# Kernel optimization log

Measured on AMD Instinct MI355X. Metric: run time of the kernel, lower is better.

## Reference

```python
import jax, jax.numpy as jnp
import numpy as np
import itertools

# Fixed 3x5 signal matrix from the module
_M = jnp.array([[1., 0., 0., 0., 0.],
                [0., 0., 1., 1., -1.],
                [0., 1., 0., -1., 1.]], dtype=jnp.float32)
# All 6 permutations of 3 elements (itertools order, matching torch code)
_PERM = jnp.array(list(itertools.permutations(range(3))), dtype=jnp.int32)  # [6,3]

B, DIN, G = 8192, 3072, 1024  # dout = 3*G = 3072


def setup_inputs() -> dict:
    key = jax.random.key(0)
    k1, k2, k3, k4 = jax.random.split(key, 4)
    x = jax.random.normal(k1, (B, DIN), dtype=jnp.float32)
    connections = jax.random.randint(k2, (G, 3), 0, DIN)  # int indices into din
    selector = jax.random.normal(k3, (G, 3), dtype=jnp.float32)
    wgts = jax.random.normal(k4, (G, 6), dtype=jnp.float32)
    return {"x": x, "connections": connections, "selector": selector, "wgts": wgts}


def reference(x, connections, selector, wgts):
    # 1. gather 3 inputs per gate: [B, G, 3]
    inputs = jnp.take(x, connections, axis=1)
    # 2. soft selector blend (training path)
    C = selector / (1.0 + jnp.abs(selector))           # [G, 3]
    absC = jnp.abs(C)
    gated = (1.0 - absC)[None] * inputs + ((C + absC) * 0.5)[None]  # [B, G, 3]
    # 3-4. all 6 permutations of the 3 gate inputs: [B, G, 6, 3]
    p = gated[:, :, _PERM]
    # 5. interaction columns -> [B, G, 6, 5]
    feat = jnp.concatenate([
        p,
        (p[..., 0] * p[..., 1])[..., None],
        (p[..., 0] * p[..., 2])[..., None],
    ], axis=-1)
    # 6-7. Signals = M @ feat^T over last dims: [B, G, 3, 6]
    signals = jnp.einsum('ms,bgps->bgmp', _M, feat)
    # 8. softmax-weighted sum over the 6 permutations: [B, G, 3]
    w = jax.nn.softmax(wgts, axis=1)                   # [G, 6]
    out = jnp.einsum('bgmp,gp->bgm', signals, w)
    # 10. flatten to [B, 3*G] = [B, dout]
    return out.reshape(out.shape[0], -1)
```

## Files before the change

### kernel.cpp

```cpp
#include <hip/hip_runtime.h>

#define G_ 1024
#define DIN_ 3072
#define B_ 8192
#define TB 4
#define RT 2
#define TPB 256

__global__ __launch_bounds__(256) void fredkin_coef_kernel(
    const int* __restrict__ conn, const float* __restrict__ sel,
    const float* __restrict__ wg, float* __restrict__ coef)
{
    int g = blockIdx.x * blockDim.x + threadIdx.x;
    if (g >= G_) return;

    float u[3], v[3];
#pragma unroll
    for (int i = 0; i < 3; ++i) {
        float s = sel[g * 3 + i];
        float C = s / (1.0f + fabsf(s));
        float a = fabsf(C);
        u[i] = 1.0f - a;
        v[i] = 0.5f * (C + a);
    }

    float w[6];
    float mx = -1e30f;
#pragma unroll
    for (int p = 0; p < 6; ++p) mx = fmaxf(mx, wg[g * 6 + p]);
    float sum = 0.0f;
#pragma unroll
    for (int p = 0; p < 6; ++p) { w[p] = expf(wg[g * 6 + p] - mx); sum += w[p]; }
    float inv = 1.0f / sum;
#pragma unroll
    for (int p = 0; p < 6; ++p) w[p] *= inv;

    const int P[6][3] = {{0,1,2},{0,2,1},{1,0,2},{1,2,0},{2,0,1},{2,1,0}};
    float L[3][3] = {{0.f,0.f,0.f},{0.f,0.f,0.f},{0.f,0.f,0.f}};
    float Q[3][3] = {{0.f,0.f,0.f},{0.f,0.f,0.f},{0.f,0.f,0.f}};
#pragma unroll
    for (int p = 0; p < 6; ++p) {
        int i0 = P[p][0], i1 = P[p][1], i2 = P[p][2];
        float wp = w[p];
        int p01 = i0 + i1 - 1;
        int p02 = i0 + i2 - 1;
        L[0][i0] += wp;
        L[1][i2] += wp; Q[1][p01] += wp; Q[1][p02] -= wp;
        L[2][i1] += wp; Q[2][p01] -= wp; Q[2][p02] += wp;
    }

#pragma unroll
    for (int m = 0; m < 3; ++m) {
        float K = L[m][0]*v[0] + L[m][1]*v[1] + L[m][2]*v[2]
                + Q[m][0]*v[0]*v[1] + Q[m][1]*v[0]*v[2] + Q[m][2]*v[1]*v[2];
        float cx0 = u[0]*(L[m][0] + Q[m][0]*v[1] + Q[m][1]*v[2]);
        float cx1 = u[1]*(L[m][1] + Q[m][0]*v[0] + Q[m][2]*v[2]);
        float cx2 = u[2]*(L[m][2] + Q[m][1]*v[0] + Q[m][2]*v[1]);
        float* om = coef + (size_t)g * 24 + m * 8;
        om[0]=K; om[1]=cx0; om[2]=cx1; om[3]=cx2;
        om[4]=Q[m][0]*u[0]*u[1]; om[5]=Q[m][1]*u[0]*u[2]; om[6]=Q[m][2]*u[1]*u[2];
        om[7]=0.f;
    }
}

__global__ __launch_bounds__(TPB) void fredkin_main_kernel(
    const float* __restrict__ x, const int* __restrict__ conn,
    const float* __restrict__ coef, float* __restrict__ out)
{
    __shared__ float xs[TB * DIN_];
    const int t = threadIdx.x;

    int c0[4], c1[4], c2[4];
#pragma unroll
    for (int gi = 0; gi < 4; ++gi) {
        const int g = t + gi * TPB;
        c0[gi] = conn[g * 3 + 0];
        c1[gi] = conn[g * 3 + 1];
        c2[gi] = conn[g * 3 + 2];
    }

    for (int tile = 0; tile < RT; ++tile) {
        const int row0 = (blockIdx.x * RT + tile) * TB;
        if (tile) __syncthreads();

        const float4* xv = (const float4*)(x + (size_t)row0 * DIN_);
        float4* sv = (float4*)xs;
#pragma unroll
        for (int i = 0; i < (TB * DIN_ / 4) / TPB; ++i) {
            __builtin_amdgcn_global_load_lds(
                (const __attribute__((address_space(1))) void*)(xv + t + i * TPB),
                (__attribute__((address_space(3))) void*)(sv + t + i * TPB),
                16, 0, 0);
        }
        __syncthreads();

#pragma unroll 2
        for (int gi = 0; gi < 4; ++gi) {
            const int g = t + gi * TPB;
            const float4* cf = (const float4*)(coef + (size_t)g * 24);
            const float4 a0 = cf[0], q0 = cf[1];
            const float4 a1 = cf[2], q1 = cf[3];
            const float4 a2 = cf[4], q2 = cf[5];
            float g0[TB], g1[TB], g2[TB];
#pragma unroll
            for (int r = 0; r < TB; ++r) {
                g0[r] = xs[r * DIN_ + c0[gi]];
                g1[r] = xs[r * DIN_ + c1[gi]];
                g2[r] = xs[r * DIN_ + c2[gi]];
            }
#pragma unroll
            for (int r = 0; r < TB; ++r) {
                const float x0 = g0[r], x1 = g1[r], x2 = g2[r];
                const float p01 = x0 * x1, p02 = x0 * x2, p12 = x1 * x2;
                float o0 = a0.x + a0.y*x0 + a0.z*x1 + a0.w*x2 + q0.x*p01 + q0.y*p02 + q0.z*p12;
                float o1 = a1.x + a1.y*x0 + a1.z*x1 + a1.w*x2 + q1.x*p01 + q1.y*p02 + q1.z*p12;
                float o2 = a2.x + a2.y*x0 + a2.z*x1 + a2.w*x2 + q2.x*p01 + q2.y*p02 + q2.z*p12;
                const size_t off = (size_t)(row0 + r) * (3 * G_) + 3 * g;
                out[off + 0] = o0;
                out[off + 1] = o1;
                out[off + 2] = o2;
            }
        }
    }
}

extern "C" void kernel_launch(void* const* d_in, const int* in_sizes, int n_in,
                              void* d_out, int out_size, void* d_ws, size_t ws_size,
                              hipStream_t stream) {
    const float* x    = (const float*)d_in[0];
    const int*   conn = (const int*)d_in[1];
    const float* sel  = (const float*)d_in[2];
    const float* wg   = (const float*)d_in[3];
    float* out  = (float*)d_out;
    float* coef = (float*)d_ws;

    hipLaunchKernelGGL(fredkin_coef_kernel, dim3(G_ / 256), dim3(256), 0, stream,
                       conn, sel, wg, coef);
    hipLaunchKernelGGL(fredkin_main_kernel, dim3(B_ / (TB * RT)), dim3(TPB), 0, stream,
                       x, conn, coef, out);
}
```

Before: 43.04 us.

## Double-buffer LDS row tiles and use nontemporal output stores

Splits the main kernel's per-block work into four 2-row tiles and double-buffers them in shared memory. The next tile's global-to-LDS load is issued while the current tile is computed, so load latency overlaps with compute. Output writes become nontemporal stores to reduce cache pollution, and launch bounds now request 3 blocks per SM. Shared memory per block stays the same. The kernel is already close to memory-bandwidth bound, so the overlap may buy little, and the smaller tiles mean more barriers per block.

```diff
diff --git a/kernel.cpp b/kernel.cpp
--- a/kernel.cpp
+++ b/kernel.cpp
@@ -3,9 +3,10 @@
 #define G_ 1024
 #define DIN_ 3072
 #define B_ 8192
-#define TB 4
-#define RT 2
+#define TB 2
+#define RT 4
 #define TPB 256
+#define GPT 4
 
 __global__ __launch_bounds__(256) void fredkin_coef_kernel(
     const int* __restrict__ conn, const float* __restrict__ sel,
@@ -63,39 +64,55 @@
     }
 }
 
-__global__ __launch_bounds__(TPB) void fredkin_main_kernel(
+__global__ __launch_bounds__(TPB, 3) void fredkin_main_kernel(
     const float* __restrict__ x, const int* __restrict__ conn,
     const float* __restrict__ coef, float* __restrict__ out)
 {
-    __shared__ float xs[TB * DIN_];
+    __shared__ float xs[2][TB * DIN_];
     const int t = threadIdx.x;
 
-    int c0[4], c1[4], c2[4];
+    int c0[GPT], c1[GPT], c2[GPT];
 #pragma unroll
-    for (int gi = 0; gi < 4; ++gi) {
+    for (int gi = 0; gi < GPT; ++gi) {
         const int g = t + gi * TPB;
         c0[gi] = conn[g * 3 + 0];
         c1[gi] = conn[g * 3 + 1];
         c2[gi] = conn[g * 3 + 2];
     }
 
-    for (int tile = 0; tile < RT; ++tile) {
-        const int row0 = (blockIdx.x * RT + tile) * TB;
-        if (tile) __syncthreads();
+    const int tile0 = blockIdx.x * RT;
 
-        const float4* xv = (const float4*)(x + (size_t)row0 * DIN_);
-        float4* sv = (float4*)xs;
+    {
+        const float4* xv = (const float4*)(x + (size_t)tile0 * TB * DIN_);
+        float4* sv = (float4*)xs[0];
 #pragma unroll
-        for (int i = 0; i < (TB * DIN_ / 4) / TPB; ++i) {
+        for (int i = 0; i < (TB * DIN_ / 4) / TPB; ++i)
             __builtin_amdgcn_global_load_lds(
                 (const __attribute__((address_space(1))) void*)(xv + t + i * TPB),
                 (__attribute__((address_space(3))) void*)(sv + t + i * TPB),
                 16, 0, 0);
+    }
+    __syncthreads();
+
+    for (int tt = 0; tt < RT; ++tt) {
+        const int cur = tt & 1;
+
+        if (tt + 1 < RT) {
+            const float4* xv =
+                (const float4*)(x + (size_t)(tile0 + tt + 1) * TB * DIN_);
+            float4* sv = (float4*)xs[cur ^ 1];
+#pragma unroll
+            for (int i = 0; i < (TB * DIN_ / 4) / TPB; ++i)
+                __builtin_amdgcn_global_load_lds(
+                    (const __attribute__((address_space(1))) void*)(xv + t + i * TPB),
+                    (__attribute__((address_space(3))) void*)(sv + t + i * TPB),
+                    16, 0, 0);
         }
-        __syncthreads();
 
-#pragma unroll 2
-        for (int gi = 0; gi < 4; ++gi) {
+        const float* xb = xs[cur];
+        const int row0 = (tile0 + tt) * TB;
+#pragma unroll
+        for (int gi = 0; gi < GPT; ++gi) {
             const int g = t + gi * TPB;
             const float4* cf = (const float4*)(coef + (size_t)g * 24);
             const float4 a0 = cf[0], q0 = cf[1];
@@ -104,9 +121,9 @@
             float g0[TB], g1[TB], g2[TB];
 #pragma unroll
             for (int r = 0; r < TB; ++r) {
-                g0[r] = xs[r * DIN_ + c0[gi]];
-                g1[r] = xs[r * DIN_ + c1[gi]];
-                g2[r] = xs[r * DIN_ + c2[gi]];
+                g0[r] = xb[r * DIN_ + c0[gi]];
+                g1[r] = xb[r * DIN_ + c1[gi]];
+                g2[r] = xb[r * DIN_ + c2[gi]];
             }
 #pragma unroll
             for (int r = 0; r < TB; ++r) {
@@ -115,12 +132,13 @@
                 float o0 = a0.x + a0.y*x0 + a0.z*x1 + a0.w*x2 + q0.x*p01 + q0.y*p02 + q0.z*p12;
                 float o1 = a1.x + a1.y*x0 + a1.z*x1 + a1.w*x2 + q1.x*p01 + q1.y*p02 + q1.z*p12;
                 float o2 = a2.x + a2.y*x0 + a2.z*x1 + a2.w*x2 + q2.x*p01 + q2.y*p02 + q2.z*p12;
-                const size_t off = (size_t)(row0 + r) * (3 * G_) + 3 * g;
-                out[off + 0] = o0;
-                out[off + 1] = o1;
-                out[off + 2] = o2;
+                float* op = out + (size_t)(row0 + r) * (3 * G_) + 3 * g;
+                __builtin_nontemporal_store(o0, op + 0);
+                __builtin_nontemporal_store(o1, op + 1);
+                __builtin_nontemporal_store(o2, op + 2);
             }
         }
+        if (tt + 1 < RT) __syncthreads();
     }
 }
 
```

After: 57.26 us. 33.0% more time.
